# Optimization experiments

Hardware: AMD Instinct MI355X
Metric: run time of the kernel (lower is better)

The kernel has to match this reference:

```python
import jax, jax.numpy as jnp
import numpy as np

H = W = 64      # input_resolution
WS = 8          # window_size
NH = 8          # num_heads
C = 256         # dim
HD = C // NH    # head_dim
SCALE = HD ** -0.5
N = WS * WS     # tokens per window
EPS = 1e-5


def _layernorm(x, g, b):
    m = jnp.mean(x, axis=-1, keepdims=True)
    v = jnp.var(x, axis=-1, keepdims=True)
    return (x - m) * jax.lax.rsqrt(v + EPS) * g + b


def _rel_pos_index():
    # Swin relative position index for a WSxWS window -> (N, N) int array
    coords = np.stack(np.meshgrid(np.arange(WS), np.arange(WS), indexing='ij'))  # (2,WS,WS)
    cf = coords.reshape(2, -1)                      # (2, N)
    rel = cf[:, :, None] - cf[:, None, :]           # (2, N, N)
    rel = rel.transpose(1, 2, 0).astype(np.int64)   # (N, N, 2)
    rel[:, :, 0] += WS - 1
    rel[:, :, 1] += WS - 1
    rel[:, :, 0] *= 2 * WS - 1
    return jnp.asarray(rel.sum(-1))                 # (N, N)


def _window_partition(x, B):
    # x: (B, H, W, C) -> (B*nW, N, C)
    x = x.reshape(B, H // WS, WS, W // WS, WS, C)
    x = x.transpose(0, 1, 3, 2, 4, 5)
    return x.reshape(-1, N, C)


def setup_inputs() -> dict:
    key = jax.random.key(0)
    ks = jax.random.split(key, 8)
    B = 16
    std = 0.02
    return {
        'x1': jax.random.normal(ks[0], (B, H * W, C), jnp.float32),
        'x2': jax.random.normal(ks[1], (B, H * W, C), jnp.float32),
        'norm1_g': jnp.ones((C,), jnp.float32),
        'norm1_b': jnp.zeros((C,), jnp.float32),
        'q_w': jax.random.normal(ks[2], (C, C), jnp.float32) * std,
        'q_b': jnp.zeros((C,), jnp.float32),
        'kv_w': jax.random.normal(ks[3], (C, 2 * C), jnp.float32) * std,
        'kv_b': jnp.zeros((2 * C,), jnp.float32),
        'proj_w': jax.random.normal(ks[4], (C, C), jnp.float32) * std,
        'proj_b': jnp.zeros((C,), jnp.float32),
        'rel_table': jax.random.normal(ks[5], ((2 * WS - 1) ** 2, NH), jnp.float32) * std,
        'norm3_g': jnp.ones((C,), jnp.float32),
        'norm3_b': jnp.zeros((C,), jnp.float32),
        'fc1_w': jax.random.normal(ks[6], (C, 4 * C), jnp.float32) * std,
        'fc1_b': jnp.zeros((4 * C,), jnp.float32),
        'fc2_w': jax.random.normal(ks[7], (4 * C, C), jnp.float32) * std,
        'fc2_b': jnp.zeros((C,), jnp.float32),
    }


def reference(x1, x2, norm1_g, norm1_b, q_w, q_b, kv_w, kv_b, proj_w, proj_b,
              rel_table, norm3_g, norm3_b, fc1_w, fc1_b, fc2_w, fc2_b):
    B = x1.shape[0]
    shortcut = x1
    # norm1 applied to both streams (as in source)
    x1n = _layernorm(x1, norm1_g, norm1_b).reshape(B, H, W, C)
    x2n = _layernorm(x2, norm1_g, norm1_b).reshape(B, H, W, C)
    x1w = _window_partition(x1n, B)  # (B_, N, C)
    x2w = _window_partition(x2n, B)  # (B_, N, C)
    B_ = x1w.shape[0]

    q = (x1w @ q_w + q_b).reshape(B_, N, NH, HD).transpose(0, 2, 1, 3)      # (B_,h,N,d)
    kv = (x2w @ kv_w + kv_b).reshape(B_, N, 2, NH, HD)
    k = kv[:, :, 0].transpose(0, 2, 1, 3)                                    # (B_,h,N,d)
    v = kv[:, :, 1].transpose(0, 2, 1, 3)                                    # (B_,h,N,d)

    attn = jnp.einsum('bhnd,bhmd->bhnm', q * SCALE, k)                       # (B_,h,N,N)
    bias = rel_table[_rel_pos_index().reshape(-1)].reshape(N, N, NH)
    attn = jax.nn.softmax(attn + bias.transpose(2, 0, 1)[None], axis=-1)

    out = jnp.einsum('bhnm,bhmd->bhnd', attn, v)
    out = out.transpose(0, 2, 1, 3).reshape(B_, N, C) @ proj_w + proj_b      # (B_,N,C)

    # window reverse -> (B, H*W, C)
    xr = out.reshape(B, H // WS, W // WS, WS, WS, C)
    xr = xr.transpose(0, 1, 3, 2, 4, 5).reshape(B, H * W, C)

    x = shortcut + xr
    h = _layernorm(x, norm3_g, norm3_b)
    h = jax.nn.gelu(h @ fc1_w + fc1_b, approximate=False) @ fc2_w + fc2_b
    return x + h
```

## Files before the change

kernel.cpp:

```cpp
#include <hip/hip_runtime.h>

typedef __bf16 bf16x8 __attribute__((ext_vector_type(8)));
typedef float f32x4 __attribute__((ext_vector_type(4)));
using u16 = unsigned short;

#define SCALE 0.17677669529663689f
#define XROW 528

__device__ __forceinline__ u16 f2bf(float f) {
    union { float f; unsigned u; } x; x.f = f;
    unsigned r = x.u + 0x7fffu + ((x.u >> 16) & 1u);
    return (u16)(r >> 16);
}
__device__ __forceinline__ unsigned pk2(float a, float b) {
    return (unsigned)f2bf(a) | ((unsigned)f2bf(b) << 16);
}
__device__ __forceinline__ float bf2f(u16 h) {
    union { unsigned u; float f; } x; x.u = ((unsigned)h) << 16; return x.f;
}
__device__ __forceinline__ float gelu_s(float x) {
    float u = 1.5957691216057308f * x * (1.f + 0.044715f * x * x);
    float e = __expf(-u);
    return x / (1.f + e);
}

__global__ __launch_bounds__(256) void prep_k(
    const float* __restrict__ q_w, const float* __restrict__ kv_w,
    const float* __restrict__ p_w, const float* __restrict__ f1w,
    const float* __restrict__ f2w, const float* __restrict__ rel,
    u16* __restrict__ qp, u16* __restrict__ kvp, u16* __restrict__ pp,
    u16* __restrict__ f1p, u16* __restrict__ f2p, float* __restrict__ biasF)
{
    int t = blockIdx.x * 256 + threadIdx.x;
    if (t < 65536) {
        int u = t;
        int e = u & 7, l = (u >> 3) & 63, ks = (u >> 9) & 7, ng = u >> 12;
        int k = ks * 32 + (l >> 4) * 8 + e;
        int n = ng * 16 + (l & 15);
        qp[u] = f2bf(q_w[k * 256 + n]);
    } else if (t < 196608) {
        int u = t - 65536;
        int e = u & 7, l = (u >> 3) & 63, ks = (u >> 9) & 7, ng = u >> 12;
        int k = ks * 32 + (l >> 4) * 8 + e;
        int n = ng * 16 + (l & 15);
        kvp[u] = f2bf(kv_w[k * 512 + n]);
    } else if (t < 262144) {
        int u = t - 196608;
        int e = u & 7, l = (u >> 3) & 63, ks = (u >> 9) & 7, ng = u >> 12;
        int k = ks * 32 + (l >> 4) * 8 + e;
        int n = ng * 16 + (l & 15);
        pp[u] = f2bf(p_w[k * 256 + n]);
    } else if (t < 524288) {
        int u = t - 262144;
        int e = u & 7, l = (u >> 3) & 63, ks = (u >> 9) & 7, ng = u >> 12;
        int k = ks * 32 + (l >> 4) * 8 + e;
        int n = ng * 16 + (l & 15);
        f1p[u] = f2bf(f1w[k * 1024 + n]);
    } else if (t < 786432) {
        int u = t - 524288;
        int e = u & 7, l = (u >> 3) & 63, ks = (u >> 9) & 31, ng = u >> 14;
        int k = ks * 32 + (l >> 4) * 8 + e;
        int n = ng * 16 + (l & 15);
        f2p[u] = f2bf(f2w[k * 256 + n]);
    } else if (t < 819200) {
        int u = t - 786432;
        int r = u & 3, l = (u >> 2) & 63, fr = (u >> 8) & 15, h = u >> 12;
        int fi = fr >> 2, fj = fr & 3;
        int m = fi * 16 + (l & 15);
        int n = fj * 16 + 4 * (l >> 4) + r;
        int idx = ((m >> 3) - (n >> 3) + 7) * 15 + ((m & 7) - (n & 7) + 7);
        biasF[u] = rel[idx * 8 + h];
    }
}

__global__ __launch_bounds__(512, 3) void attn_mega(
    const float* __restrict__ x1, const float* __restrict__ x2,
    const float* __restrict__ gw, const float* __restrict__ bw,
    const bf16x8* __restrict__ qp, const bf16x8* __restrict__ kvp,
    const float* __restrict__ q_b, const float* __restrict__ kv_b,
    const float* __restrict__ biasF, const bf16x8* __restrict__ pp,
    const float* __restrict__ p_b, u16* __restrict__ xbw)
{
    __shared__ __align__(16) char SMEM[74752];
    u16* Xl0  = (u16*)SMEM;
    u16* Xl1  = (u16*)(SMEM + 33792);
    u16* VtA  = (u16*)SMEM;
    u16* Olds = (u16*)(SMEM + 40960);
    const int t = threadIdx.x, lane = t & 63, w = t >> 6;
    const int g = lane >> 4, c = lane & 15;
    const int win = blockIdx.x;
    const int b_ = win >> 6, wh = (win >> 3) & 7, ww = win & 7;

    {
        float4 gg = *(const float4*)(gw + lane * 4);
        float4 bb = *(const float4*)(bw + lane * 4);
        for (int it = 0; it < 16; it++) {
            int idx = w * 16 + it;
            int st = idx >> 6, n = idx & 63;
            const float* src = st ? x2 : x1;
            size_t srow = (size_t)b_ * 4096 + (wh * 8 + (n >> 3)) * 64 + ww * 8 + (n & 7);
            float4 v = *(const float4*)(src + srow * 256 + lane * 4);
            float s = v.x + v.y + v.z + v.w;
            float q = v.x * v.x + v.y * v.y + v.z * v.z + v.w * v.w;
            #pragma unroll
            for (int m = 1; m < 64; m <<= 1) {
                s += __shfl_xor(s, m, 64);
                q += __shfl_xor(q, m, 64);
            }
            float mean = s * (1.0f / 256.0f);
            float var  = q * (1.0f / 256.0f) - mean * mean;
            float rstd = rsqrtf(var + 1e-5f);
            float n0 = (v.x - mean) * rstd * gg.x + bb.x;
            float n1 = (v.y - mean) * rstd * gg.y + bb.y;
            float n2 = (v.z - mean) * rstd * gg.z + bb.z;
            float n3 = (v.w - mean) * rstd * gg.w + bb.w;
            uint2 pk = { pk2(n0, n1), pk2(n2, n3) };
            u16* dst = st ? Xl1 : Xl0;
            *(uint2*)((char*)dst + n * XROW + lane * 8) = pk;
        }
    }
    __syncthreads();

    const int srcA = c + 16 * ((2 * g) & 3);
    const int srcB = srcA + 16;
    const bool nhi = (g >= 2);

#define GEMM256(acc, WPTR, NGBASE, XSRC)                                      \
    { _Pragma("unroll")                                                       \
      for (int i = 0; i < 4; i++) { acc[i][0] = (f32x4){0,0,0,0};             \
                                    acc[i][1] = (f32x4){0,0,0,0}; }           \
      _Pragma("unroll")                                                       \
      for (int ks = 0; ks < 8; ks++) {                                        \
          bf16x8 wf[2], af[4];                                                \
          _Pragma("unroll")                                                   \
          for (int n = 0; n < 2; n++)                                         \
              wf[n] = WPTR[(size_t)(((NGBASE) + n) * 8 + ks) * 64 + lane];    \
          _Pragma("unroll")                                                   \
          for (int i = 0; i < 4; i++)                                         \
              af[i] = *(const bf16x8*)((char*)XSRC + (i * 16 + c) * XROW      \
                                       + g * 16 + ks * 64);                   \
          __builtin_amdgcn_s_setprio(1);                                      \
          _Pragma("unroll")                                                   \
          for (int i = 0; i < 4; i++)                                         \
              _Pragma("unroll")                                               \
              for (int n = 0; n < 2; n++)                                     \
                  acc[i][n] = __builtin_amdgcn_mfma_f32_16x16x32_bf16(        \
                      wf[n], af[i], acc[i][n], 0, 0, 0);                      \
          __builtin_amdgcn_s_setprio(0);                                      \
      } }

#define ADDBIAS(acc, BPTR, CBASE)                                             \
    { _Pragma("unroll")                                                       \
      for (int i = 0; i < 4; i++)                                             \
          _Pragma("unroll")                                                   \
          for (int n = 0; n < 2; n++) {                                       \
              float4 b4 = *(const float4*)((BPTR) + (CBASE) + n * 16 + 4 * g);\
              acc[i][n][0] += b4.x; acc[i][n][1] += b4.y;                     \
              acc[i][n][2] += b4.z; acc[i][n][3] += b4.w;                     \
          } }

#define REPACK(acc, frag)                                                     \
    { unsigned w0_[4][2], w1_[4][2];                                          \
      _Pragma("unroll")                                                       \
      for (int i = 0; i < 4; i++)                                             \
          _Pragma("unroll")                                                   \
          for (int n = 0; n < 2; n++) {                                       \
              w0_[i][n] = pk2(acc[i][n][0], acc[i][n][1]);                    \
              w1_[i][n] = pk2(acc[i][n][2], acc[i][n][3]);                    \
          }                                                                   \
      _Pragma("unroll")                                                       \
      for (int i = 0; i < 4; i++) {                                           \
          unsigned x0a = __shfl(w0_[i][0], srcA), x0b = __shfl(w0_[i][1], srcA);\
          unsigned y0a = __shfl(w1_[i][0], srcA), y0b = __shfl(w1_[i][1], srcA);\
          unsigned x1a = __shfl(w0_[i][0], srcB), x1b = __shfl(w0_[i][1], srcB);\
          unsigned y1a = __shfl(w1_[i][0], srcB), y1b = __shfl(w1_[i][1], srcB);\
          union { uint4 u; bf16x8 v; } cv;                                    \
          cv.u.x = nhi ? x0b : x0a;                                           \
          cv.u.y = nhi ? y0b : y0a;                                           \
          cv.u.z = nhi ? x1b : x1a;                                           \
          cv.u.w = nhi ? y1b : y1a;                                           \
          frag[i] = cv.v;                                                     \
      } }

    bf16x8 qf[4], kf[4];
    f32x4 av[4][2];
    {
        f32x4 acc[4][2];
        GEMM256(acc, kvp, 2 * w, Xl1)
        ADDBIAS(acc, kv_b, w * 32)
        REPACK(acc, kf)
        GEMM256(acc, qp, 2 * w, Xl0)
        ADDBIAS(acc, q_b, w * 32)
        REPACK(acc, qf)
        GEMM256(av, kvp, 16 + 2 * w, Xl1)
        ADDBIAS(av, kv_b, 256 + w * 32)
    }
    __syncthreads();

    u16* vt = VtA + w * 32 * 80;
    #pragma unroll
    for (int i = 0; i < 4; i++)
        #pragma unroll
        for (int n = 0; n < 2; n++)
            #pragma unroll
            for (int r = 0; r < 4; r++)
                vt[(n * 16 + 4 * g + r) * 80 + i * 16 + c] = f2bf(av[i][n][r]);

    f32x4 s[4][4];
    #pragma unroll
    for (int i = 0; i < 4; i++)
        #pragma unroll
        for (int j = 0; j < 4; j++) {
            s[i][j] = (f32x4){0.f, 0.f, 0.f, 0.f};
            s[i][j] = __builtin_amdgcn_mfma_f32_16x16x32_bf16(kf[j], qf[i], s[i][j], 0, 0, 0);
        }

    #pragma unroll
    for (int i = 0; i < 4; i++)
        #pragma unroll
        for (int j = 0; j < 4; j++) {
            f32x4 bf4 = *(const f32x4*)(biasF + ((size_t)(w * 16 + i * 4 + j) * 64 + lane) * 4);
            #pragma unroll
            for (int r = 0; r < 4; r++) s[i][j][r] = s[i][j][r] * SCALE + bf4[r];
        }

    #pragma unroll
    for (int i = 0; i < 4; i++) {
        float mx = -1e30f;
        #pragma unroll
        for (int j = 0; j < 4; j++)
            #pragma unroll
            for (int r = 0; r < 4; r++) mx = fmaxf(mx, s[i][j][r]);
        mx = fmaxf(mx, __shfl_xor(mx, 16, 64));
        mx = fmaxf(mx, __shfl_xor(mx, 32, 64));
        float sum = 0.f;
        #pragma unroll
        for (int j = 0; j < 4; j++)
            #pragma unroll
            for (int r = 0; r < 4; r++) {
                float e = __expf(s[i][j][r] - mx);
                s[i][j][r] = e; sum += e;
            }
        sum += __shfl_xor(sum, 16, 64);
        sum += __shfl_xor(sum, 32, 64);
        float inv = 1.f / sum;
        #pragma unroll
        for (int j = 0; j < 4; j++)
            #pragma unroll
            for (int r = 0; r < 4; r++) s[i][j][r] *= inv;
    }

    unsigned pw0[4][4], pw1[4][4];
    #pragma unroll
    for (int i = 0; i < 4; i++)
        #pragma unroll
        for (int j = 0; j < 4; j++) {
            pw0[i][j] = pk2(s[i][j][0], s[i][j][1]);
            pw1[i][j] = pk2(s[i][j][2], s[i][j][3]);
        }
    f32x4 o[4][2];
    #pragma unroll
    for (int i = 0; i < 4; i++) { o[i][0] = (f32x4){0,0,0,0}; o[i][1] = (f32x4){0,0,0,0}; }
    #pragma unroll
    for (int ks = 0; ks < 2; ks++) {
        bf16x8 pa[4], vb[2];
        #pragma unroll
        for (int i = 0; i < 4; i++) {
            unsigned a0 = __shfl(pw0[i][2 * ks], srcA), b0 = __shfl(pw0[i][2 * ks + 1], srcA);
            unsigned a1 = __shfl(pw1[i][2 * ks], srcA), b1 = __shfl(pw1[i][2 * ks + 1], srcA);
            unsigned a2 = __shfl(pw0[i][2 * ks], srcB), b2 = __shfl(pw0[i][2 * ks + 1], srcB);
            unsigned a3 = __shfl(pw1[i][2 * ks], srcB), b3 = __shfl(pw1[i][2 * ks + 1], srcB);
            union { uint4 u; bf16x8 v; } cv;
            cv.u.x = nhi ? b0 : a0;
            cv.u.y = nhi ? b1 : a1;
            cv.u.z = nhi ? b2 : a2;
            cv.u.w = nhi ? b3 : a3;
            pa[i] = cv.v;
        }
        #pragma unroll
        for (int j = 0; j < 2; j++) {
            int d = j * 16 + c;
            vb[j] = *(const bf16x8*)(vt + d * 80 + ks * 32 + 8 * g);
        }
        #pragma unroll
        for (int i = 0; i < 4; i++)
            #pragma unroll
            for (int j = 0; j < 2; j++)
                o[i][j] = __builtin_amdgcn_mfma_f32_16x16x32_bf16(vb[j], pa[i], o[i][j], 0, 0, 0);
    }

    #pragma unroll
    for (int i = 0; i < 4; i++) {
        int row = i * 16 + c;
        #pragma unroll
        for (int j = 0; j < 2; j++) {
            uint2 pk = { pk2(o[i][j][0], o[i][j][1]), pk2(o[i][j][2], o[i][j][3]) };
            *(uint2*)((char*)Olds + row * XROW + w * 64 + j * 32 + g * 8) = pk;
        }
    }
    __syncthreads();

    f32x4 ap[4][2];
    #pragma unroll
    for (int i = 0; i < 4; i++) { ap[i][0] = (f32x4){0,0,0,0}; ap[i][1] = (f32x4){0,0,0,0}; }
    #pragma unroll
    for (int ks = 0; ks < 8; ks++) {
        bf16x8 wf[2], ah[4];
        #pragma unroll
        for (int n = 0; n < 2; n++)
            wf[n] = pp[(size_t)((w * 2 + n) * 8 + ks) * 64 + lane];
        #pragma unroll
        for (int i = 0; i < 4; i++)
            ah[i] = *(const bf16x8*)((char*)Olds + (i * 16 + c) * XROW
                                     + g * 16 + ks * 64);
        __builtin_amdgcn_s_setprio(1);
        #pragma unroll
        for (int i = 0; i < 4; i++)
            #pragma unroll
            for (int n = 0; n < 2; n++)
                ap[i][n] = __builtin_amdgcn_mfma_f32_16x16x32_bf16(
                    wf[n], ah[i], ap[i][n], 0, 0, 0);
        __builtin_amdgcn_s_setprio(0);
    }

    #pragma unroll
    for (int i = 0; i < 4; i++) {
        int n = i * 16 + c;
        size_t nrow = (size_t)b_ * 4096 + (wh * 8 + (n >> 3)) * 64 + ww * 8 + (n & 7);
        #pragma unroll
        for (int j = 0; j < 2; j++) {
            int col = w * 32 + j * 16 + 4 * g;
            float4 b4 = *(const float4*)(p_b + col);
            float4 r4 = *(const float4*)(x1 + nrow * 256 + col);
            uint2 pk = { pk2(ap[i][j][0] + b4.x + r4.x, ap[i][j][1] + b4.y + r4.y),
                         pk2(ap[i][j][2] + b4.z + r4.z, ap[i][j][3] + b4.w + r4.w) };
            *(uint2*)(xbw + nrow * 256 + col) = pk;
        }
    }
#undef GEMM256
#undef ADDBIAS
#undef REPACK
}

__global__ __launch_bounds__(512, 4) void mlp_mega(
    const u16* __restrict__ xb, const float* __restrict__ gw,
    const float* __restrict__ bw, const bf16x8* __restrict__ f1p,
    const bf16x8* __restrict__ f2p, const float* __restrict__ f1b,
    const float* __restrict__ f2b, float* __restrict__ out)
{
    __shared__ __align__(16) u16 Xl[64 * 264];
    __shared__ __align__(16) u16 Hl[64 * 264];
    const int t = threadIdx.x, lane = t & 63, w = t >> 6;
    const int g = lane >> 4, c = lane & 15;
    const int m0 = blockIdx.x * 64;

    {
        float4 gg = *(const float4*)(gw + lane * 4);
        float4 bb = *(const float4*)(bw + lane * 4);
        for (int it = 0; it < 8; it++) {
            int row = w * 8 + it;
            uint2 rv = *(const uint2*)(xb + (size_t)(m0 + row) * 256 + lane * 4);
            float v0 = bf2f((u16)rv.x), v1 = bf2f((u16)(rv.x >> 16));
            float v2 = bf2f((u16)rv.y), v3 = bf2f((u16)(rv.y >> 16));
            float s = v0 + v1 + v2 + v3;
            float q = v0 * v0 + v1 * v1 + v2 * v2 + v3 * v3;
            #pragma unroll
            for (int m = 1; m < 64; m <<= 1) {
                s += __shfl_xor(s, m, 64);
                q += __shfl_xor(q, m, 64);
            }
            float mean = s * (1.0f / 256.0f);
            float var  = q * (1.0f / 256.0f) - mean * mean;
            float rstd = rsqrtf(var + 1e-5f);
            float n0 = (v0 - mean) * rstd * gg.x + bb.x;
            float n1 = (v1 - mean) * rstd * gg.y + bb.y;
            float n2 = (v2 - mean) * rstd * gg.z + bb.z;
            float n3 = (v3 - mean) * rstd * gg.w + bb.w;
            uint2 pk = { pk2(n0, n1), pk2(n2, n3) };
            *(uint2*)((char*)Xl + row * XROW + lane * 8) = pk;
        }
    }
    __syncthreads();

    f32x4 acc2[4][2];
    #pragma unroll
    for (int i = 0; i < 4; i++) { acc2[i][0] = (f32x4){0,0,0,0}; acc2[i][1] = (f32x4){0,0,0,0}; }

    #pragma unroll
    for (int hc = 0; hc < 4; hc++) {
        f32x4 acc1[4][2];
        #pragma unroll
        for (int i = 0; i < 4; i++) { acc1[i][0] = (f32x4){0,0,0,0}; acc1[i][1] = (f32x4){0,0,0,0}; }

        const bf16x8* f1base = f1p + (size_t)((hc * 16 + w * 2) * 8) * 64 + lane;
        bf16x8 wA[2], wB[2];
        #pragma unroll
        for (int n = 0; n < 2; n++) wA[n] = f1base[(n * 8 + 0) * 64];

#define FC1_STEP(WREG, ks_)                                                   \
        {                                                                     \
            bf16x8 af[4];                                                     \
            _Pragma("unroll")                                                 \
            for (int i = 0; i < 4; i++)                                       \
                af[i] = *(const bf16x8*)((char*)Xl + (i * 16 + c) * XROW      \
                                         + g * 16 + (ks_) * 64);             \
            __builtin_amdgcn_s_setprio(1);                                    \
            _Pragma("unroll")                                                 \
            for (int i = 0; i < 4; i++)                                       \
                _Pragma("unroll")                                             \
                for (int n = 0; n < 2; n++)                                   \
                    acc1[i][n] = __builtin_amdgcn_mfma_f32_16x16x32_bf16(     \
                        WREG[n], af[i], acc1[i][n], 0, 0, 0);                 \
            __builtin_amdgcn_s_setprio(0);                                    \
        }

        #pragma unroll
        for (int ks = 0; ks < 8; ks += 2) {
            #pragma unroll
            for (int n = 0; n < 2; n++) wB[n] = f1base[(n * 8 + ks + 1) * 64];
            FC1_STEP(wA, ks)
            if (ks + 2 < 8) {
                #pragma unroll
                for (int n = 0; n < 2; n++) wA[n] = f1base[(n * 8 + ks + 2) * 64];
            }
            FC1_STEP(wB, ks + 1)
        }
#undef FC1_STEP

        #pragma unroll
        for (int i = 0; i < 4; i++) {
            int row = i * 16 + c;
            #pragma unroll
            for (int n = 0; n < 2; n++) {
                float4 b4 = *(const float4*)(f1b + hc * 256 + w * 32 + n * 16 + 4 * g);
                float h0 = gelu_s(acc1[i][n][0] + b4.x);
                float h1 = gelu_s(acc1[i][n][1] + b4.y);
                float h2 = gelu_s(acc1[i][n][2] + b4.z);
                float h3 = gelu_s(acc1[i][n][3] + b4.w);
                uint2 pk = { pk2(h0, h1), pk2(h2, h3) };
                *(uint2*)((char*)Hl + row * XROW + w * 64 + n * 32 + g * 8) = pk;
            }
        }
        __syncthreads();

        const bf16x8* f2base = f2p + (size_t)((w * 2) * 32 + hc * 8) * 64 + lane;
        #pragma unroll
        for (int n = 0; n < 2; n++) wA[n] = f2base[(n * 32 + 0) * 64];

#define FC2_STEP(WREG, ks_)                                                   \
        {                                                                     \
            bf16x8 ah[4];                                                     \
            _Pragma("unroll")                                                 \
            for (int i = 0; i < 4; i++)                                       \
                ah[i] = *(const bf16x8*)((char*)Hl + (i * 16 + c) * XROW      \
                                         + g * 16 + (ks_) * 64);             \
            __builtin_amdgcn_s_setprio(1);                                    \
            _Pragma("unroll")                                                 \
            for (int i = 0; i < 4; i++)                                       \
                _Pragma("unroll")                                             \
                for (int n = 0; n < 2; n++)                                   \
                    acc2[i][n] = __builtin_amdgcn_mfma_f32_16x16x32_bf16(     \
                        WREG[n], ah[i], acc2[i][n], 0, 0, 0);                 \
            __builtin_amdgcn_s_setprio(0);                                    \
        }

        #pragma unroll
        for (int ks = 0; ks < 8; ks += 2) {
            #pragma unroll
            for (int n = 0; n < 2; n++) wB[n] = f2base[(n * 32 + ks + 1) * 64];
            FC2_STEP(wA, ks)
            if (ks + 2 < 8) {
                #pragma unroll
                for (int n = 0; n < 2; n++) wA[n] = f2base[(n * 32 + ks + 2) * 64];
            }
            FC2_STEP(wB, ks + 1)
        }
#undef FC2_STEP
        __syncthreads();
    }

    #pragma unroll
    for (int i = 0; i < 4; i++) {
        int row = m0 + i * 16 + c;
        #pragma unroll
        for (int n = 0; n < 2; n++) {
            int col = w * 32 + n * 16 + 4 * g;
            float4 b4 = *(const float4*)(f2b + col);
            uint2 rr = *(const uint2*)(xb + (size_t)row * 256 + col);
            float4 ov = { acc2[i][n][0] + b4.x + bf2f((u16)rr.x),
                          acc2[i][n][1] + b4.y + bf2f((u16)(rr.x >> 16)),
                          acc2[i][n][2] + b4.z + bf2f((u16)rr.y),
                          acc2[i][n][3] + b4.w + bf2f((u16)(rr.y >> 16)) };
            *(float4*)(out + (size_t)row * 256 + col) = ov;
        }
    }
}

extern "C" void kernel_launch(void* const* d_in, const int* in_sizes, int n_in,
                              void* d_out, int out_size, void* d_ws, size_t ws_size,
                              hipStream_t stream)
{
    const float* x1  = (const float*)d_in[0];
    const float* x2  = (const float*)d_in[1];
    const float* n1g = (const float*)d_in[2];
    const float* n1b = (const float*)d_in[3];
    const float* q_w = (const float*)d_in[4];
    const float* q_b = (const float*)d_in[5];
    const float* kv_w= (const float*)d_in[6];
    const float* kv_b= (const float*)d_in[7];
    const float* p_w = (const float*)d_in[8];
    const float* p_b = (const float*)d_in[9];
    const float* rel = (const float*)d_in[10];
    const float* n3g = (const float*)d_in[11];
    const float* n3b = (const float*)d_in[12];
    const float* f1w = (const float*)d_in[13];
    const float* f1b = (const float*)d_in[14];
    const float* f2w = (const float*)d_in[15];
    const float* f2b = (const float*)d_in[16];

    char* ws = (char*)d_ws;
    u16*   qp    = (u16*)(ws + 0);
    u16*   kvp   = (u16*)(ws + 131072);
    u16*   pp    = (u16*)(ws + 393216);
    u16*   f1p   = (u16*)(ws + 524288);
    u16*   f2p   = (u16*)(ws + 1048576);
    float* biasF = (float*)(ws + 1572864);
    u16*   xbw   = (u16*)(ws + 2097152);

    float* out = (float*)d_out;

    prep_k<<<3200, 256, 0, stream>>>(q_w, kv_w, p_w, f1w, f2w, rel,
                                     qp, kvp, pp, f1p, f2p, biasF);
    attn_mega<<<1024, 512, 0, stream>>>(x1, x2, n1g, n1b, (const bf16x8*)qp,
                                        (const bf16x8*)kvp, q_b, kv_b, biasF,
                                        (const bf16x8*)pp, p_b, xbw);
    mlp_mega<<<1024, 512, 0, stream>>>(xbw, n3g, n3b, (const bf16x8*)f1p,
                                       (const bf16x8*)f2p, f1b, f2b, out);
}
```

Baseline: 241.6 us.

## Process four LayerNorm rows per wavefront and use native bf16 conversion

The LayerNorm prologues in both attention and MLP kernels now split each wavefront into four 16-lane groups, with each lane holding 16 channels. This cuts the shuffle reduction from six steps to four and processes four rows per iteration with wider 16-byte loads and stores. The manual round-to-nearest bf16 conversion is replaced with the compiler's native __bf16 cast, which may map to hardware convert instructions. GELU now uses exp2f with a pre-scaled constant. Global load coalescing changes because each lane reads 64 contiguous bytes instead of 16.

After: 222.7 us. 1.09x faster.

```diff
diff --git a/kernel.cpp b/kernel.cpp
--- a/kernel.cpp
+++ b/kernel.cpp
@@ -8,19 +8,18 @@
 #define XROW 528
 
 __device__ __forceinline__ u16 f2bf(float f) {
-    union { float f; unsigned u; } x; x.f = f;
-    unsigned r = x.u + 0x7fffu + ((x.u >> 16) & 1u);
-    return (u16)(r >> 16);
+    union { __bf16 h; u16 u; } x; x.h = (__bf16)f; return x.u;
 }
 __device__ __forceinline__ unsigned pk2(float a, float b) {
-    return (unsigned)f2bf(a) | ((unsigned)f2bf(b) << 16);
+    union { struct { __bf16 lo, hi; } s; unsigned u; } x;
+    x.s.lo = (__bf16)a; x.s.hi = (__bf16)b; return x.u;
 }
 __device__ __forceinline__ float bf2f(u16 h) {
     union { unsigned u; float f; } x; x.u = ((unsigned)h) << 16; return x.f;
 }
 __device__ __forceinline__ float gelu_s(float x) {
-    float u = 1.5957691216057308f * x * (1.f + 0.044715f * x * x);
-    float e = __expf(-u);
+    float u = 2.3022150048054216f * x * (1.f + 0.044715f * x * x);
+    float e = exp2f(-u);
     return x / (1.f + e);
 }
 
@@ -73,6 +72,37 @@
     }
 }
 
+#define LN_ROW16(SRCP, GG, BB, OUT0, OUT1)                                    \
+    {                                                                         \
+        float4 v0 = *(const float4*)(SRCP);                                   \
+        float4 v1 = *(const float4*)(SRCP + 4);                               \
+        float4 v2 = *(const float4*)(SRCP + 8);                               \
+        float4 v3 = *(const float4*)(SRCP + 12);                              \
+        float s = (v0.x + v0.y + v0.z + v0.w) + (v1.x + v1.y + v1.z + v1.w)   \
+                + (v2.x + v2.y + v2.z + v2.w) + (v3.x + v3.y + v3.z + v3.w);  \
+        float q = v0.x*v0.x + v0.y*v0.y + v0.z*v0.z + v0.w*v0.w               \
+                + v1.x*v1.x + v1.y*v1.y + v1.z*v1.z + v1.w*v1.w               \
+                + v2.x*v2.x + v2.y*v2.y + v2.z*v2.z + v2.w*v2.w               \
+                + v3.x*v3.x + v3.y*v3.y + v3.z*v3.z + v3.w*v3.w;              \
+        _Pragma("unroll")                                                     \
+        for (int m_ = 1; m_ <= 8; m_ <<= 1) {                                 \
+            s += __shfl_xor(s, m_, 64);                                       \
+            q += __shfl_xor(q, m_, 64);                                       \
+        }                                                                     \
+        float mean = s * (1.0f / 256.0f);                                     \
+        float rstd = rsqrtf(q * (1.0f / 256.0f) - mean * mean + 1e-5f);       \
+        uint4 o0_, o1_;                                                       \
+        o0_.x = pk2((v0.x-mean)*rstd*GG[0].x+BB[0].x, (v0.y-mean)*rstd*GG[0].y+BB[0].y); \
+        o0_.y = pk2((v0.z-mean)*rstd*GG[0].z+BB[0].z, (v0.w-mean)*rstd*GG[0].w+BB[0].w); \
+        o0_.z = pk2((v1.x-mean)*rstd*GG[1].x+BB[1].x, (v1.y-mean)*rstd*GG[1].y+BB[1].y); \
+        o0_.w = pk2((v1.z-mean)*rstd*GG[1].z+BB[1].z, (v1.w-mean)*rstd*GG[1].w+BB[1].w); \
+        o1_.x = pk2((v2.x-mean)*rstd*GG[2].x+BB[2].x, (v2.y-mean)*rstd*GG[2].y+BB[2].y); \
+        o1_.y = pk2((v2.z-mean)*rstd*GG[2].z+BB[2].z, (v2.w-mean)*rstd*GG[2].w+BB[2].w); \
+        o1_.z = pk2((v3.x-mean)*rstd*GG[3].x+BB[3].x, (v3.y-mean)*rstd*GG[3].y+BB[3].y); \
+        o1_.w = pk2((v3.z-mean)*rstd*GG[3].z+BB[3].z, (v3.w-mean)*rstd*GG[3].w+BB[3].w); \
+        OUT0 = o0_; OUT1 = o1_;                                               \
+    }
+
 __global__ __launch_bounds__(512, 3) void attn_mega(
     const float* __restrict__ x1, const float* __restrict__ x2,
     const float* __restrict__ gw, const float* __restrict__ bw,
@@ -92,31 +122,26 @@
     const int b_ = win >> 6, wh = (win >> 3) & 7, ww = win & 7;
 
     {
-        float4 gg = *(const float4*)(gw + lane * 4);
-        float4 bb = *(const float4*)(bw + lane * 4);
-        for (int it = 0; it < 16; it++) {
-            int idx = w * 16 + it;
+        const int ln_sub = lane >> 4, ln_c = lane & 15;
+        float4 GG[4], BB[4];
+        #pragma unroll
+        for (int j = 0; j < 4; j++) {
+            GG[j] = *(const float4*)(gw + ln_c * 16 + j * 4);
+            BB[j] = *(const float4*)(bw + ln_c * 16 + j * 4);
+        }
+        #pragma unroll
+        for (int it = 0; it < 4; it++) {
+            int idx = w * 16 + it * 4 + ln_sub;
             int st = idx >> 6, n = idx & 63;
             const float* src = st ? x2 : x1;
             size_t srow = (size_t)b_ * 4096 + (wh * 8 + (n >> 3)) * 64 + ww * 8 + (n & 7);
-            float4 v = *(const float4*)(src + srow * 256 + lane * 4);
-            float s = v.x + v.y + v.z + v.w;
-            float q = v.x * v.x + v.y * v.y + v.z * v.z + v.w * v.w;
-            #pragma unroll
-            for (int m = 1; m < 64; m <<= 1) {
-                s += __shfl_xor(s, m, 64);
-                q += __shfl_xor(q, m, 64);
-            }
-            float mean = s * (1.0f / 256.0f);
-            float var  = q * (1.0f / 256.0f) - mean * mean;
-            float rstd = rsqrtf(var + 1e-5f);
-            float n0 = (v.x - mean) * rstd * gg.x + bb.x;
-            float n1 = (v.y - mean) * rstd * gg.y + bb.y;
-            float n2 = (v.z - mean) * rstd * gg.z + bb.z;
-            float n3 = (v.w - mean) * rstd * gg.w + bb.w;
-            uint2 pk = { pk2(n0, n1), pk2(n2, n3) };
+            const float* p = src + srow * 256 + ln_c * 16;
+            uint4 o0, o1;
+            LN_ROW16(p, GG, BB, o0, o1)
             u16* dst = st ? Xl1 : Xl0;
-            *(uint2*)((char*)dst + n * XROW + lane * 8) = pk;
+            char* base = (char*)dst + n * XROW + ln_c * 32;
+            *(uint4*)(base) = o0;
+            *(uint4*)(base + 16) = o1;
         }
     }
     __syncthreads();
@@ -355,29 +380,52 @@
     const int m0 = blockIdx.x * 64;
 
     {
-        float4 gg = *(const float4*)(gw + lane * 4);
-        float4 bb = *(const float4*)(bw + lane * 4);
-        for (int it = 0; it < 8; it++) {
-            int row = w * 8 + it;
-            uint2 rv = *(const uint2*)(xb + (size_t)(m0 + row) * 256 + lane * 4);
-            float v0 = bf2f((u16)rv.x), v1 = bf2f((u16)(rv.x >> 16));
-            float v2 = bf2f((u16)rv.y), v3 = bf2f((u16)(rv.y >> 16));
-            float s = v0 + v1 + v2 + v3;
-            float q = v0 * v0 + v1 * v1 + v2 * v2 + v3 * v3;
-            #pragma unroll
-            for (int m = 1; m < 64; m <<= 1) {
-                s += __shfl_xor(s, m, 64);
-                q += __shfl_xor(q, m, 64);
+        const int ln_sub = lane >> 4, ln_c = lane & 15;
+        float4 GG[4], BB[4];
+        #pragma unroll
+        for (int j = 0; j < 4; j++) {
+            GG[j] = *(const float4*)(gw + ln_c * 16 + j * 4);
+            BB[j] = *(const float4*)(bw + ln_c * 16 + j * 4);
+        }
+        #pragma unroll
+        for (int it = 0; it < 2; it++) {
+            int row = w * 8 + it * 4 + ln_sub;
+            const u16* p = xb + (size_t)(m0 + row) * 256 + ln_c * 16;
+            uint4 rv = *(const uint4*)(p);
+            uint4 rw = *(const uint4*)(p + 8);
+            float v[16];
+            v[0] = bf2f((u16)rv.x);  v[1] = bf2f((u16)(rv.x >> 16));
+            v[2] = bf2f((u16)rv.y);  v[3] = bf2f((u16)(rv.y >> 16));
+            v[4] = bf2f((u16)rv.z);  v[5] = bf2f((u16)(rv.z >> 16));
+            v[6] = bf2f((u16)rv.w);  v[7] = bf2f((u16)(rv.w >> 16));
+            v[8] = bf2f((u16)rw.x);  v[9] = bf2f((u16)(rw.x >> 16));
+            v[10] = bf2f((u16)rw.y); v[11] = bf2f((u16)(rw.y >> 16));
+            v[12] = bf2f((u16)rw.z); v[13] = bf2f((u16)(rw.z >> 16));
+            v[14] = bf2f((u16)rw.w); v[15] = bf2f((u16)(rw.w >> 16));
+            float s = 0.f, q = 0.f;
+            #pragma unroll
+            for (int e = 0; e < 16; e++) { s += v[e]; q += v[e] * v[e]; }
+            #pragma unroll
+            for (int m_ = 1; m_ <= 8; m_ <<= 1) {
+                s += __shfl_xor(s, m_, 64);
+                q += __shfl_xor(q, m_, 64);
             }
             float mean = s * (1.0f / 256.0f);
-            float var  = q * (1.0f / 256.0f) - mean * mean;
-            float rstd = rsqrtf(var + 1e-5f);
-            float n0 = (v0 - mean) * rstd * gg.x + bb.x;
-            float n1 = (v1 - mean) * rstd * gg.y + bb.y;
-            float n2 = (v2 - mean) * rstd * gg.z + bb.z;
-            float n3 = (v3 - mean) * rstd * gg.w + bb.w;
-            uint2 pk = { pk2(n0, n1), pk2(n2, n3) };
-            *(uint2*)((char*)Xl + row * XROW + lane * 8) = pk;
+            float rstd = rsqrtf(q * (1.0f / 256.0f) - mean * mean + 1e-5f);
+            uint4 o0, o1;
+            const float* G = (const float*)GG;
+            const float* B = (const float*)BB;
+            o0.x = pk2((v[0]-mean)*rstd*G[0]+B[0],  (v[1]-mean)*rstd*G[1]+B[1]);
+            o0.y = pk2((v[2]-mean)*rstd*G[2]+B[2],  (v[3]-mean)*rstd*G[3]+B[3]);
+            o0.z = pk2((v[4]-mean)*rstd*G[4]+B[4],  (v[5]-mean)*rstd*G[5]+B[5]);
+            o0.w = pk2((v[6]-mean)*rstd*G[6]+B[6],  (v[7]-mean)*rstd*G[7]+B[7]);
+            o1.x = pk2((v[8]-mean)*rstd*G[8]+B[8],  (v[9]-mean)*rstd*G[9]+B[9]);
+            o1.y = pk2((v[10]-mean)*rstd*G[10]+B[10],(v[11]-mean)*rstd*G[11]+B[11]);
+            o1.z = pk2((v[12]-mean)*rstd*G[12]+B[12],(v[13]-mean)*rstd*G[13]+B[13]);
+            o1.w = pk2((v[14]-mean)*rstd*G[14]+B[14],(v[15]-mean)*rstd*G[15]+B[15]);
+            char* base = (char*)Xl + row * XROW + ln_c * 32;
+            *(uint4*)(base) = o0;
+            *(uint4*)(base + 16) = o1;
         }
     }
     __syncthreads();
```
